# Performance work log

Hardware: AMD Instinct MI355X
Metric: run time of the kernel (lower is better)

## Reference

```python
import jax, jax.numpy as jnp
import numpy as np

ALPHA = 0.9
BETA = 0.85
THRESHOLD = 0.1
SURR_SCALE = 100.0  # SpyTorch-style surrogate gradient scale


@jax.custom_vjp
def surr_spike(x):
    # Heaviside forward, surrogate gradient backward (SurrGradSpike)
    return (x > 0.0).astype(x.dtype)


def _surr_fwd(x):
    return surr_spike(x), x


def _surr_bwd(x, g):
    return (g / (SURR_SCALE * jnp.abs(x) + 1.0) ** 2,)


surr_spike.defvjp(_surr_fwd, _surr_bwd)


def setup_inputs() -> dict:
    key = jax.random.key(0)
    k1, k2, k3 = jax.random.split(key, 3)
    B, T, D_IN, N = 64, 256, 512, 1024
    inputs = jax.random.normal(k1, (B, T, D_IN), dtype=jnp.float32)
    weights = 0.1 * jax.random.normal(k2, (D_IN, N), dtype=jnp.float32)
    recurrent_weights = 0.1 * jax.random.normal(k3, (N, N), dtype=jnp.float32)
    return {"inputs": inputs, "weights": weights, "recurrent_weights": recurrent_weights}


def reference(inputs, weights, recurrent_weights):
    B, T, D_IN = inputs.shape
    N = weights.shape[1]

    def step(carry, x_t):
        mem, syn, spk = carry
        h = jnp.einsum('bd,dn->bn', x_t, weights)          # input projection
        rec_h = jnp.einsum('bn,nm->bm', spk, recurrent_weights)  # recurrent drive
        new_syn = ALPHA * syn + h + rec_h
        new_mem = BETA * mem + new_syn
        mthr = new_mem - THRESHOLD
        out = surr_spike(mthr)
        new_mem = jnp.where(mthr > 0.0, jnp.zeros_like(new_mem), new_mem)  # reset
        return (new_mem, new_syn, out), (out, new_mem, new_syn)

    zeros = jnp.zeros((B, N), dtype=inputs.dtype)
    init = (zeros, zeros, zeros)
    x_tbd = jnp.transpose(inputs, (1, 0, 2))  # [T, B, D]
    (mem, syn, spk), (spk_rec, mem_rec, syn_rec) = jax.lax.scan(step, init, x_tbd)
    # back to [B, T, N]
    spk_rec = jnp.transpose(spk_rec, (1, 0, 2))
    mem_rec = jnp.transpose(mem_rec, (1, 0, 2))
    syn_rec = jnp.transpose(syn_rec, (1, 0, 2))
    return (spk_rec, (mem, syn, spk), (mem_rec, syn_rec))
```

## Files before the change

kernel.cpp:

```cpp
#include <hip/hip_runtime.h>

typedef __attribute__((ext_vector_type(8))) _Float16 f16x8;
typedef __attribute__((ext_vector_type(4))) float f32x4;

static constexpr int   B_  = 64;
static constexpr int   T_  = 256;
static constexpr int   D_  = 512;
static constexpr int   N_  = 1024;
static constexpr float ALPHA_ = 0.9f;
static constexpr float BETA_  = 0.85f;
static constexpr float THR_   = 0.1f;

__global__ __launch_bounds__(256) void dsrnn_hgemm(const float* __restrict__ X,
                                                   const float* __restrict__ W,
                                                   float* __restrict__ H) {
  __shared__ float As[16][128];
  __shared__ float Bs[16][128];
  const int tid = threadIdx.x;
  const int nb  = blockIdx.x & 7;
  const int mb  = blockIdx.x >> 3;
  const int r0  = mb << 7;
  const int n0  = nb << 7;

  float acc[8][8];
#pragma unroll
  for (int i = 0; i < 8; ++i)
#pragma unroll
    for (int j = 0; j < 8; ++j) acc[i][j] = 0.f;

  for (int k0 = 0; k0 < D_; k0 += 16) {
#pragma unroll
    for (int i = 0; i < 2; ++i) {
      const int f   = tid * 2 + i;
      const int row = f >> 2;
      const int kq  = (f & 3) << 2;
      const float4 v =
          *reinterpret_cast<const float4*>(&X[(size_t)(r0 + row) * D_ + k0 + kq]);
      As[kq + 0][row] = v.x;
      As[kq + 1][row] = v.y;
      As[kq + 2][row] = v.z;
      As[kq + 3][row] = v.w;
    }
#pragma unroll
    for (int i = 0; i < 2; ++i) {
      const int f  = tid * 2 + i;
      const int kr = f >> 5;
      const int c  = (f & 31) << 2;
      *reinterpret_cast<float4*>(&Bs[kr][c]) =
          *reinterpret_cast<const float4*>(&W[(size_t)(k0 + kr) * N_ + n0 + c]);
    }
    __syncthreads();
    const int ty = tid >> 4, tx = tid & 15;
#pragma unroll
    for (int kk = 0; kk < 16; ++kk) {
      float a[8], b[8];
      *reinterpret_cast<float4*>(&a[0]) = *reinterpret_cast<const float4*>(&As[kk][ty * 8]);
      *reinterpret_cast<float4*>(&a[4]) = *reinterpret_cast<const float4*>(&As[kk][ty * 8 + 4]);
      *reinterpret_cast<float4*>(&b[0]) = *reinterpret_cast<const float4*>(&Bs[kk][tx * 8]);
      *reinterpret_cast<float4*>(&b[4]) = *reinterpret_cast<const float4*>(&Bs[kk][tx * 8 + 4]);
#pragma unroll
      for (int i = 0; i < 8; ++i)
#pragma unroll
        for (int j = 0; j < 8; ++j) acc[i][j] = fmaf(a[i], b[j], acc[i][j]);
    }
    __syncthreads();
  }
  const int ty = tid >> 4, tx = tid & 15;
#pragma unroll
  for (int i = 0; i < 8; ++i) {
    const size_t r = (size_t)(r0 + ty * 8 + i);
#pragma unroll
    for (int j = 0; j < 8; j += 4)
      *reinterpret_cast<float4*>(&H[r * N_ + n0 + tx * 8 + j]) =
          *reinterpret_cast<const float4*>(&acc[i][j]);
  }
}

__global__ __launch_bounds__(256, 1) void dsrnn_step7(
    const float* __restrict__ Rw,
    float* __restrict__ spk_rec,
    float* __restrict__ mem_rec,
    float* __restrict__ syn_rec,
    float* __restrict__ mem_fin,
    float* __restrict__ syn_fin,
    float* __restrict__ spk_fin,
    unsigned long long* masks)
{
  extern __shared__ unsigned char RsB[];
  __shared__ unsigned smaskU[16][33];
  __shared__ float scratch[4][512];

  const int tid  = threadIdx.x;
  const int bq   = blockIdx.x >> 5;
  const int mg   = blockIdx.x & 31;
  const int wv   = tid >> 6;
  const int lane = tid & 63;
  const int kg   = lane >> 4;
  const int cc   = lane & 15;

  for (int k = 0; k < 128; ++k) {
    const int e  = (k << 8) + tid;
    const int n  = e >> 5;
    const int ml = e & 31;
    const float v = Rw[(size_t)n * N_ + (mg << 5) + ml];
    const _Float16 hi = (_Float16)v;
    const float hif = (float)hi;
    const _Float16 lo = (_Float16)((v - hif) * 4096.0f);
    const int s   = n >> 5;
    const int kin = n & 31;
    const int ln  = ((kin >> 3) << 4) + (ml & 15);
    const int mt  = ml >> 4;
    const int off = ((((s << 1) + mt) << 1) << 10) + (ln << 4) + ((kin & 7) << 1);
    *(_Float16*)(RsB + off)        = hi;
    *(_Float16*)(RsB + off + 1024) = lo;
  }

  const int bl1 = tid >> 5;
  const int bl2 = bl1 + 8;
  const int ml_ = tid & 31;
  const int b1  = (bq << 4) + bl1;
  const int b2  = (bq << 4) + bl2;
  const int m   = (mg << 5) + ml_;

  float mem1 = 0.f, syn1 = 0.f, spv1 = 0.f;
  float mem2 = 0.f, syn2 = 0.f, spv2 = 0.f;

  __syncthreads();

  for (int t = 0; t < T_; ++t) {
    const size_t i1 = ((size_t)b1 * T_ + t) * N_ + m;
    const size_t i2 = ((size_t)b2 * T_ + t) * N_ + m;
    const float h1 = syn_rec[i1];
    const float h2 = syn_rec[i2];

    {
      unsigned long long* base = masks + (size_t)(t & 1) * 2048;
      unsigned long long* p1 = base + (size_t)b1 * 32 + ml_;
      unsigned long long* p2 = base + (size_t)b2 * 32 + ml_;
      unsigned long long w1 =
          __hip_atomic_load(p1, __ATOMIC_RELAXED, __HIP_MEMORY_SCOPE_AGENT);
      int g = 0;
      while ((unsigned)(w1 >> 32) != (unsigned)t && ++g < (1 << 20)) {
        __builtin_amdgcn_s_sleep(1);
        w1 = __hip_atomic_load(p1, __ATOMIC_RELAXED, __HIP_MEMORY_SCOPE_AGENT);
      }
      unsigned long long w2 =
          __hip_atomic_load(p2, __ATOMIC_RELAXED, __HIP_MEMORY_SCOPE_AGENT);
      g = 0;
      while ((unsigned)(w2 >> 32) != (unsigned)t && ++g < (1 << 20)) {
        __builtin_amdgcn_s_sleep(1);
        w2 = __hip_atomic_load(p2, __ATOMIC_RELAXED, __HIP_MEMORY_SCOPE_AGENT);
      }
      smaskU[bl1][ml_] = (unsigned)w1;
      smaskU[bl2][ml_] = (unsigned)w2;
    }
    __syncthreads();

    f32x4 c0h = {0.f, 0.f, 0.f, 0.f};
    f32x4 c0l = {0.f, 0.f, 0.f, 0.f};
    f32x4 c1h = {0.f, 0.f, 0.f, 0.f};
    f32x4 c1l = {0.f, 0.f, 0.f, 0.f};
    const int shB = kg << 3;
#pragma unroll
    for (int ss = 0; ss < 8; ++ss) {
      const int s = (wv << 3) + ss;
      const unsigned bits8 = (smaskU[cc][s] >> shB) & 0xFFu;
      union { unsigned u[4]; f16x8 v; } A;
#pragma unroll
      for (int p = 0; p < 4; ++p) {
        const unsigned e0 = (bits8 >> (2 * p)) & 1u;
        const unsigned e1 = (bits8 >> (2 * p + 1)) & 1u;
        A.u[p] = e0 * 0x3C00u + e1 * 0x3C000000u;
      }
      const unsigned char* sb = RsB + (s << 12) + (lane << 4);
      const f16x8 b00 = *reinterpret_cast<const f16x8*>(sb);
      const f16x8 b01 = *reinterpret_cast<const f16x8*>(sb + 1024);
      const f16x8 b10 = *reinterpret_cast<const f16x8*>(sb + 2048);
      const f16x8 b11 = *reinterpret_cast<const f16x8*>(sb + 3072);
      c0h = __builtin_amdgcn_mfma_f32_16x16x32_f16(A.v, b00, c0h, 0, 0, 0);
      c0l = __builtin_amdgcn_mfma_f32_16x16x32_f16(A.v, b01, c0l, 0, 0, 0);
      c1h = __builtin_amdgcn_mfma_f32_16x16x32_f16(A.v, b10, c1h, 0, 0, 0);
      c1l = __builtin_amdgcn_mfma_f32_16x16x32_f16(A.v, b11, c1l, 0, 0, 0);
    }
    constexpr float INV4096 = 1.0f / 4096.0f;
#pragma unroll
    for (int r = 0; r < 4; ++r) {
      const int row = (kg << 2) + r;
      scratch[wv][(row << 5) + cc]      = fmaf(c0l[r], INV4096, c0h[r]);
      scratch[wv][(row << 5) + cc + 16] = fmaf(c1l[r], INV4096, c1h[r]);
    }
    __syncthreads();

    const int o1 = (bl1 << 5) + ml_;
    const int o2 = (bl2 << 5) + ml_;
    const float rec1 =
        scratch[0][o1] + scratch[1][o1] + scratch[2][o1] + scratch[3][o1];
    const float rec2 =
        scratch[0][o2] + scratch[1][o2] + scratch[2][o2] + scratch[3][o2];

    syn1 = ALPHA_ * syn1 + h1 + rec1;
    mem1 = BETA_ * mem1 + syn1;
    const bool sp1 = (mem1 - THR_) > 0.f;
    spv1 = sp1 ? 1.f : 0.f;
    mem1 = sp1 ? 0.f : mem1;

    syn2 = ALPHA_ * syn2 + h2 + rec2;
    mem2 = BETA_ * mem2 + syn2;
    const bool sp2 = (mem2 - THR_) > 0.f;
    spv2 = sp2 ? 1.f : 0.f;
    mem2 = sp2 ? 0.f : mem2;

    const unsigned long long ball1 = __ballot(sp1);
    const unsigned long long ball2 = __ballot(sp2);
    if (ml_ == 0) {
      const unsigned sh = lane & 32;
      const unsigned long long tag = ((unsigned long long)(unsigned)(t + 1)) << 32;
      unsigned long long* nb = masks + (size_t)((t + 1) & 1) * 2048;
      __hip_atomic_store(nb + (size_t)b1 * 32 + mg,
                         tag | (unsigned)(ball1 >> sh),
                         __ATOMIC_RELAXED, __HIP_MEMORY_SCOPE_AGENT);
      __hip_atomic_store(nb + (size_t)b2 * 32 + mg,
                         tag | (unsigned)(ball2 >> sh),
                         __ATOMIC_RELAXED, __HIP_MEMORY_SCOPE_AGENT);
    }

    spk_rec[i1] = spv1; mem_rec[i1] = mem1; syn_rec[i1] = syn1;
    spk_rec[i2] = spv2; mem_rec[i2] = mem2; syn_rec[i2] = syn2;
  }

  mem_fin[b1 * N_ + m] = mem1; syn_fin[b1 * N_ + m] = syn1; spk_fin[b1 * N_ + m] = spv1;
  mem_fin[b2 * N_ + m] = mem2; syn_fin[b2 * N_ + m] = syn2; spk_fin[b2 * N_ + m] = spv2;
}

extern "C" void kernel_launch(void* const* d_in, const int* in_sizes, int n_in,
                              void* d_out, int out_size, void* d_ws, size_t ws_size,
                              hipStream_t stream) {
  const float* X  = (const float*)d_in[0];
  const float* W  = (const float*)d_in[1];
  const float* Rw = (const float*)d_in[2];

  float* out = (float*)d_out;
  const size_t BTN = (size_t)B_ * T_ * N_;
  const size_t BN  = (size_t)B_ * N_;
  float* spk_rec = out;
  float* mem_fin = out + BTN;
  float* syn_fin = mem_fin + BN;
  float* spk_fin = syn_fin + BN;
  float* mem_rec = spk_fin + BN;
  float* syn_rec = mem_rec + BTN;

  unsigned long long* masks = (unsigned long long*)d_ws;
  hipMemsetAsync(d_ws, 0, (size_t)2 * 64 * 32 * sizeof(unsigned long long), stream);

  dsrnn_hgemm<<<dim3(1024), dim3(256), 0, stream>>>(X, W, syn_rec);

  (void)hipFuncSetAttribute((const void*)dsrnn_step7,
                            hipFuncAttributeMaxDynamicSharedMemorySize, 131072);
  void* args[] = {(void*)&Rw,      (void*)&spk_rec, (void*)&mem_rec,
                  (void*)&syn_rec, (void*)&mem_fin, (void*)&syn_fin,
                  (void*)&spk_fin, (void*)&masks};
  hipLaunchCooperativeKernel((void*)dsrnn_step7, dim3(128), dim3(256), args,
                             131072, stream);
}
```

Baseline: 887.4 us.

## Poll spike masks per wavefront and distribute via shuffles, dropping LDS barrier

Each wavefront now polls only the two mask words it needs and hands them to lanes with __shfl, instead of the whole block polling into shared memory and then hitting a barrier. That removes one __syncthreads per timestep along with the smaskU LDS staging. The reduction scratch is double-buffered by timestep parity so the next step's writes cannot race the current step's reads. The sleep in the spin loop is also removed, which makes polling more aggressive and may add memory traffic.

Result: slower. 1.059 ms (+19.3%).

```diff
diff --git a/kernel.cpp b/kernel.cpp
--- a/kernel.cpp
+++ b/kernel.cpp
@@ -76,7 +76,7 @@
   }
 }
 
-__global__ __launch_bounds__(256, 1) void dsrnn_step7(
+__global__ __launch_bounds__(256, 1) void dsrnn_step8(
     const float* __restrict__ Rw,
     float* __restrict__ spk_rec,
     float* __restrict__ mem_rec,
@@ -87,8 +87,7 @@
     unsigned long long* masks)
 {
   extern __shared__ unsigned char RsB[];
-  __shared__ unsigned smaskU[16][33];
-  __shared__ float scratch[4][512];
+  __shared__ float scratch[2][4][512];
 
   const int tid  = threadIdx.x;
   const int bq   = blockIdx.x >> 5;
@@ -122,6 +121,8 @@
   const int b2  = (bq << 4) + bl2;
   const int m   = (mg << 5) + ml_;
 
+  const int pw_off = ((bq << 4) + cc) * 32 + (wv << 3) + (kg << 1);
+
   float mem1 = 0.f, syn1 = 0.f, spv1 = 0.f;
   float mem2 = 0.f, syn2 = 0.f, spv2 = 0.f;
 
@@ -133,28 +134,22 @@
     const float h1 = syn_rec[i1];
     const float h2 = syn_rec[i2];
 
+    unsigned pay0, pay1;
     {
-      unsigned long long* base = masks + (size_t)(t & 1) * 2048;
-      unsigned long long* p1 = base + (size_t)b1 * 32 + ml_;
-      unsigned long long* p2 = base + (size_t)b2 * 32 + ml_;
+      unsigned long long* p0 = masks + (size_t)(t & 1) * 2048 + pw_off;
+      unsigned long long w0 =
+          __hip_atomic_load(p0,     __ATOMIC_RELAXED, __HIP_MEMORY_SCOPE_AGENT);
       unsigned long long w1 =
-          __hip_atomic_load(p1, __ATOMIC_RELAXED, __HIP_MEMORY_SCOPE_AGENT);
+          __hip_atomic_load(p0 + 1, __ATOMIC_RELAXED, __HIP_MEMORY_SCOPE_AGENT);
       int g = 0;
-      while ((unsigned)(w1 >> 32) != (unsigned)t && ++g < (1 << 20)) {
-        __builtin_amdgcn_s_sleep(1);
-        w1 = __hip_atomic_load(p1, __ATOMIC_RELAXED, __HIP_MEMORY_SCOPE_AGENT);
+      while ((((unsigned)(w0 >> 32) != (unsigned)t) |
+              ((unsigned)(w1 >> 32) != (unsigned)t)) && ++g < (1 << 20)) {
+        w0 = __hip_atomic_load(p0,     __ATOMIC_RELAXED, __HIP_MEMORY_SCOPE_AGENT);
+        w1 = __hip_atomic_load(p0 + 1, __ATOMIC_RELAXED, __HIP_MEMORY_SCOPE_AGENT);
       }
-      unsigned long long w2 =
-          __hip_atomic_load(p2, __ATOMIC_RELAXED, __HIP_MEMORY_SCOPE_AGENT);
-      g = 0;
-      while ((unsigned)(w2 >> 32) != (unsigned)t && ++g < (1 << 20)) {
-        __builtin_amdgcn_s_sleep(1);
-        w2 = __hip_atomic_load(p2, __ATOMIC_RELAXED, __HIP_MEMORY_SCOPE_AGENT);
-      }
-      smaskU[bl1][ml_] = (unsigned)w1;
-      smaskU[bl2][ml_] = (unsigned)w2;
-    }
-    __syncthreads();
+      pay0 = (unsigned)w0;
+      pay1 = (unsigned)w1;
+    }
 
     f32x4 c0h = {0.f, 0.f, 0.f, 0.f};
     f32x4 c0l = {0.f, 0.f, 0.f, 0.f};
@@ -163,8 +158,9 @@
     const int shB = kg << 3;
 #pragma unroll
     for (int ss = 0; ss < 8; ++ss) {
-      const int s = (wv << 3) + ss;
-      const unsigned bits8 = (smaskU[cc][s] >> shB) & 0xFFu;
+      const int srcl = cc + ((ss >> 1) << 4);
+      const unsigned word = __shfl((ss & 1) ? pay1 : pay0, srcl, 64);
+      const unsigned bits8 = (word >> shB) & 0xFFu;
       union { unsigned u[4]; f16x8 v; } A;
 #pragma unroll
       for (int p = 0; p < 4; ++p) {
@@ -172,6 +168,7 @@
         const unsigned e1 = (bits8 >> (2 * p + 1)) & 1u;
         A.u[p] = e0 * 0x3C00u + e1 * 0x3C000000u;
       }
+      const int s = (wv << 3) + ss;
       const unsigned char* sb = RsB + (s << 12) + (lane << 4);
       const f16x8 b00 = *reinterpret_cast<const f16x8*>(sb);
       const f16x8 b01 = *reinterpret_cast<const f16x8*>(sb + 1024);
@@ -183,20 +180,22 @@
       c1l = __builtin_amdgcn_mfma_f32_16x16x32_f16(A.v, b11, c1l, 0, 0, 0);
     }
     constexpr float INV4096 = 1.0f / 4096.0f;
-#pragma unroll
-    for (int r = 0; r < 4; ++r) {
-      const int row = (kg << 2) + r;
-      scratch[wv][(row << 5) + cc]      = fmaf(c0l[r], INV4096, c0h[r]);
-      scratch[wv][(row << 5) + cc + 16] = fmaf(c1l[r], INV4096, c1h[r]);
+    {
+      float* scr = &scratch[t & 1][wv][0];
+#pragma unroll
+      for (int r = 0; r < 4; ++r) {
+        const int row = (kg << 2) + r;
+        scr[(row << 5) + cc]      = fmaf(c0l[r], INV4096, c0h[r]);
+        scr[(row << 5) + cc + 16] = fmaf(c1l[r], INV4096, c1h[r]);
+      }
     }
     __syncthreads();
 
+    const float* sc = &scratch[t & 1][0][0];
     const int o1 = (bl1 << 5) + ml_;
     const int o2 = (bl2 << 5) + ml_;
-    const float rec1 =
-        scratch[0][o1] + scratch[1][o1] + scratch[2][o1] + scratch[3][o1];
-    const float rec2 =
-        scratch[0][o2] + scratch[1][o2] + scratch[2][o2] + scratch[3][o2];
+    const float rec1 = sc[o1] + sc[512 + o1] + sc[1024 + o1] + sc[1536 + o1];
+    const float rec2 = sc[o2] + sc[512 + o2] + sc[1024 + o2] + sc[1536 + o2];
 
     syn1 = ALPHA_ * syn1 + h1 + rec1;
     mem1 = BETA_ * mem1 + syn1;
@@ -254,11 +253,11 @@
 
   dsrnn_hgemm<<<dim3(1024), dim3(256), 0, stream>>>(X, W, syn_rec);
 
-  (void)hipFuncSetAttribute((const void*)dsrnn_step7,
+  (void)hipFuncSetAttribute((const void*)dsrnn_step8,
                             hipFuncAttributeMaxDynamicSharedMemorySize, 131072);
   void* args[] = {(void*)&Rw,      (void*)&spk_rec, (void*)&mem_rec,
                   (void*)&syn_rec, (void*)&mem_fin, (void*)&syn_fin,
                   (void*)&spk_fin, (void*)&masks};
-  hipLaunchCooperativeKernel((void*)dsrnn_step7, dim3(128), dim3(256), args,
+  hipLaunchCooperativeKernel((void*)dsrnn_step8, dim3(128), dim3(256), args,
                              131072, stream);
 }
```
